# Optimization experiments

Hardware: AMD Instinct MI355X
Metric: run time of the kernel (lower is better)

## Reference

```python
import jax, jax.numpy as jnp
import numpy as np

BATCH, SEQ, IN_DIM, OUT_DIM, N_STATE = 16, 4096, 64, 64, 512


def setup_inputs() -> dict:
    key = jax.random.key(0)
    k_x, k_a, k_b, k_c, k_d = jax.random.split(key, 5)
    x = jax.random.normal(k_x, (BATCH, SEQ, IN_DIM), dtype=jnp.float32)
    # Stable transition matrix: spectral-norm-ish scaling keeps h bounded over SEQ steps.
    A = jax.random.normal(k_a, (N_STATE, N_STATE), dtype=jnp.float32) * (0.9 / np.sqrt(N_STATE))
    B = jax.random.normal(k_b, (N_STATE, IN_DIM), dtype=jnp.float32) / np.sqrt(IN_DIM)
    C = jax.random.normal(k_c, (OUT_DIM, N_STATE), dtype=jnp.float32) / np.sqrt(N_STATE)
    D = jax.random.normal(k_d, (OUT_DIM, IN_DIM), dtype=jnp.float32) / np.sqrt(IN_DIM)
    return {"x": x, "A": A, "B": B, "C": C, "D": D}


def reference(x, A, B, C, D):
    """Linear SSM recurrence: h_t = A h_{t-1} + B x_t ; y_t = C h_t + D x_t.

    x: [batch, seq, in_dim] -> y: [batch, seq, out_dim]
    """
    batch = x.shape[0]
    n = A.shape[0]
    # Precompute input projections once (batched GEMMs outside the scan).
    bx = jnp.einsum("ni,bsi->sbn", B, x)   # [seq, batch, n_state]
    dx = jnp.einsum("oi,bsi->bso", D, x)   # [batch, seq, out_dim]

    def step(h, bx_t):
        # h: [batch, n_state]; bx_t: [batch, n_state]
        h_new = h @ A.T + bx_t
        return h_new, h_new

    h0 = jnp.zeros((batch, n), dtype=x.dtype)
    _, hs = jax.lax.scan(step, h0, bx)      # hs: [seq, batch, n_state]
    y = jnp.einsum("on,sbn->bso", C, hs) + dx
    return y
```

## Files before the change

### kernel.cpp

```cpp
#include <hip/hip_runtime.h>
#include <cstdint>
#include <cstddef>

#define BATCH 16
#define SEQ   4096
#define NS    512
#define TLAG  96
#define CTILE 128
#define XROWS (CTILE + TLAG - 1)
#define XSTR  72
#define BLK   32768

typedef unsigned short u16;
typedef unsigned int   u32;
typedef short bf16x8 __attribute__((ext_vector_type(8)));
typedef float f32x4  __attribute__((ext_vector_type(4)));

__device__ __forceinline__ u16 f2bf(float f) {
    u32 u = __builtin_bit_cast(u32, f);
    return (u16)((u + 0x7FFFu + ((u >> 16) & 1u)) >> 16);
}
__device__ __forceinline__ float bf2f(u16 h) {
    return __builtin_bit_cast(float, (u32)h << 16);
}

__global__ __launch_bounds__(256) void prep_mat(const float* __restrict__ A,
                                                const float* __restrict__ B,
                                                const float* __restrict__ C,
                                                u16* __restrict__ Arm,
                                                u16* __restrict__ At,
                                                u16* __restrict__ Rt,
                                                u16* __restrict__ L)
{
    const int id = blockIdx.x * 256 + threadIdx.x;
    if (id < 262144) {
        const int c = id & 511;
        const u16 v = f2bf(A[id]);
        Arm[id] = v;
        At[(size_t)c * 512 + (id >> 9)] = v;
    } else if (id < 262144 + 32768) {
        const int i = id - 262144;
        Rt[(size_t)(i & 63) * 512 + (i >> 6)] = f2bf(B[i]);
    } else {
        const int i = id - 262144 - 32768;
        L[i] = f2bf(C[i]);
    }
}

__device__ __forceinline__ void gemm_tile(const u16* __restrict__ apM,
                                          const u16* __restrict__ bT, int n0,
                                          u16* __restrict__ oRM,
                                          u16* __restrict__ oT, int rowT,
                                          u16* __restrict__ lds)
{
    const int tid = threadIdx.x;
    const int w = tid >> 6, l = tid & 63;
    const int lr = l & 15, q8 = (l >> 4) * 8;

    const u16* ap  = apM + (size_t)(w * 16 + lr) * NS + q8;
    const u16* bp0 = bT  + (size_t)(n0 + lr) * NS + q8;

    f32x4 acc[4];
    const f32x4 zero = {0.f, 0.f, 0.f, 0.f};
    #pragma unroll
    for (int nt = 0; nt < 4; ++nt) acc[nt] = zero;

    #pragma unroll 4
    for (int ks = 0; ks < 16; ++ks) {
        const bf16x8 a = *(const bf16x8*)(ap + ks * 32);
        #pragma unroll
        for (int nt = 0; nt < 4; ++nt) {
            const bf16x8 bfr = *(const bf16x8*)(bp0 + (size_t)nt * 16 * NS + ks * 32);
            acc[nt] = __builtin_amdgcn_mfma_f32_16x16x32_bf16(a, bfr, acc[nt], 0, 0, 0);
        }
    }

    const int rr = (l >> 4) * 4;
    if (oT) {
        #pragma unroll
        for (int nt = 0; nt < 4; ++nt) {
            const int col = n0 + nt * 16 + lr;
            ushort4 pk;
            pk.x = f2bf(acc[nt][0]); pk.y = f2bf(acc[nt][1]);
            pk.z = f2bf(acc[nt][2]); pk.w = f2bf(acc[nt][3]);
            *(ushort4*)(oT + (size_t)col * NS + rowT + w * 16 + rr) = pk;
        }
    }
    if (oRM) {
        #pragma unroll
        for (int nt = 0; nt < 4; ++nt)
            #pragma unroll
            for (int r = 0; r < 4; ++r)
                lds[(w * 16 + rr + r) * 72 + nt * 16 + lr] = f2bf(acc[nt][r]);
        __syncthreads();
        const int r  = tid >> 2;
        const int c0 = (tid & 3) * 16;
        #pragma unroll
        for (int k = 0; k < 4; ++k) {
            const ushort4 q = *(const ushort4*)&lds[r * 72 + c0 + k * 4];
            *(ushort4*)(oRM + (size_t)r * NS + n0 + c0 + k * 4) = q;
        }
    }
}

__global__ __launch_bounds__(256, 1) void stage_kernel(const u16* __restrict__ expAp,
                                                       const u16* __restrict__ expBT,
                                                       u16* __restrict__ expOut,
                                                       const u16* __restrict__ sqIn,
                                                       const u16* __restrict__ sqInT,
                                                       u16* __restrict__ sqOutRM,
                                                       u16* __restrict__ sqOutT,
                                                       int E)
{
    __shared__ u16 lds[64 * 72];
    const int t = blockIdx.x;
    if (t < E) {
        const int j = t >> 3, n0 = (t & 7) * 64;
        gemm_tile(expAp + (size_t)j * BLK, expBT, n0,
                  expOut + (size_t)j * BLK, nullptr, 0, lds);
    } else {
        const int tt = t - E;
        const int mr = tt >> 3, n0 = (tt & 7) * 64;
        gemm_tile(sqIn + (size_t)mr * BLK, sqInT, n0,
                  sqOutRM + (size_t)mr * BLK, sqOutT, mr * 64, lds);
    }
}

__global__ __launch_bounds__(256, 1) void g_kernel(const u16* __restrict__ Rt,
                                                   const u16* __restrict__ L,
                                                   const float* __restrict__ D,
                                                   u16* __restrict__ Gsw)
{
    __shared__ u16 lds[64 * 72];
    const int m = blockIdx.x;
    const int q = m >> 4, r = m & 15;
    const u16* ap0 = Rt + (size_t)q * BLK;
    const u16* bT0 = L  + (size_t)r * BLK;

    const int tid = threadIdx.x;
    const int w = tid >> 6, l = tid & 63;
    const int lr = l & 15, q8 = (l >> 4) * 8;

    const u16* ap  = ap0 + (size_t)(w * 16 + lr) * NS + q8;
    const u16* bp0 = bT0 + (size_t)lr * NS + q8;

    f32x4 acc[4];
    const f32x4 zero = {0.f, 0.f, 0.f, 0.f};
    #pragma unroll
    for (int nt = 0; nt < 4; ++nt) acc[nt] = zero;

    #pragma unroll 4
    for (int ks = 0; ks < 16; ++ks) {
        const bf16x8 a = *(const bf16x8*)(ap + ks * 32);
        #pragma unroll
        for (int nt = 0; nt < 4; ++nt) {
            const bf16x8 bfr = *(const bf16x8*)(bp0 + (size_t)nt * 16 * NS + ks * 32);
            acc[nt] = __builtin_amdgcn_mfma_f32_16x16x32_bf16(a, bfr, acc[nt], 0, 0, 0);
        }
    }

    const int rr = (l >> 4) * 4;
    #pragma unroll
    for (int nt = 0; nt < 4; ++nt)
        #pragma unroll
        for (int rk = 0; rk < 4; ++rk)
            lds[(nt * 16 + lr) * 72 + (w * 16 + rr + rk)] = f2bf(acc[nt][rk]);
    __syncthreads();

    const int f = tid >> 6;
    #pragma unroll
    for (int f2 = 0; f2 < 8; f2 += 4) {
        const int fi = f2 + f;
        const int ks = fi >> 2, nt = fi & 3;
        const int o  = nt * 16 + (l & 15);
        const int i0 = ks * 32 + (l >> 4) * 8;
        u16 v[8];
        #pragma unroll
        for (int j = 0; j < 8; ++j) {
            u16 gv = lds[o * 72 + i0 + j];
            if (m == 0) gv = f2bf(bf2f(gv) + D[o * 64 + i0 + j]);
            v[j] = gv;
        }
        ushort4 p0; p0.x = v[0]; p0.y = v[1]; p0.z = v[2]; p0.w = v[3];
        ushort4 p1; p1.x = v[4]; p1.y = v[5]; p1.z = v[6]; p1.w = v[7];
        u16* dst = Gsw + ((size_t)(m * 8 + fi) * 64 + l) * 8;
        *(ushort4*)(dst + 0) = p0;
        *(ushort4*)(dst + 4) = p1;
    }
}

__global__ __launch_bounds__(256, 2) void conv_kernel(const float* __restrict__ x,
                                                      const u16* __restrict__ gsw,
                                                      float* __restrict__ y)
{
    __shared__ u16 Xs[XROWS * XSTR];
    __shared__ uint4 Gs[2][1024];

    const int tid = threadIdx.x;
    const int b  = blockIdx.y;
    const int t0 = blockIdx.x * CTILE;

    {
        const int g = tid & 15;
        int r = tid >> 4;
        #pragma unroll
        for (int it = 0; it < 14; ++it, r += 16) {
            if (r < XROWS) {
                const int t = t0 + r - (TLAG - 1);
                ushort4 o;
                if (t < 0) {
                    o.x = 0; o.y = 0; o.z = 0; o.w = 0;
                } else {
                    const float4 v = *(const float4*)(x + ((size_t)b * SEQ + t) * 64 + g * 4);
                    o.x = f2bf(v.x); o.y = f2bf(v.y); o.z = f2bf(v.z); o.w = f2bf(v.w);
                }
                *(ushort4*)&Xs[r * XSTR + g * 4] = o;
            }
        }
    }

    const uint4* gp4 = (const uint4*)gsw;
    uint4 st[4];
    #pragma unroll
    for (int j = 0; j < 4; ++j) st[j] = gp4[tid + j * 256];

    const int w    = tid >> 6;
    const int l    = tid & 63;
    const int lr   = l & 15;
    const int q8   = (l >> 4) * 8;
    const int wrow = w * 32;

    f32x4 acc[2][4];
    const f32x4 zero = {0.f, 0.f, 0.f, 0.f};
    #pragma unroll
    for (int mt = 0; mt < 2; ++mt)
        #pragma unroll
        for (int nt = 0; nt < 4; ++nt) acc[mt][nt] = zero;

    #pragma unroll
    for (int j = 0; j < 4; ++j) Gs[0][tid + j * 256] = st[j];
    __syncthreads();

    for (int p = 0; p < TLAG / 2; ++p) {
        const int cur = p & 1;
        if (p < TLAG / 2 - 1) {
            #pragma unroll
            for (int j = 0; j < 4; ++j) st[j] = gp4[(p + 1) * 1024 + tid + j * 256];
        }
        #pragma unroll
        for (int sub = 0; sub < 2; ++sub) {
            const int m = 2 * p + sub;
            bf16x8 bc[8];
            #pragma unroll
            for (int f = 0; f < 8; ++f)
                bc[f] = __builtin_bit_cast(bf16x8, Gs[cur][sub * 512 + f * 64 + l]);

            const int rbase = wrow + lr + (TLAG - 1) - m;
            bf16x8 a[2][2];
            #pragma unroll
            for (int mt = 0; mt < 2; ++mt)
                #pragma unroll
                for (int ks = 0; ks < 2; ++ks)
                    a[mt][ks] = *(const bf16x8*)&Xs[(rbase + mt * 16) * XSTR + ks * 32 + q8];

            #pragma unroll
            for (int ks = 0; ks < 2; ++ks)
                #pragma unroll
                for (int mt = 0; mt < 2; ++mt)
                    #pragma unroll
                    for (int nt = 0; nt < 4; ++nt)
                        acc[mt][nt] = __builtin_amdgcn_mfma_f32_16x16x32_bf16(
                            a[mt][ks], bc[ks * 4 + nt], acc[mt][nt], 0, 0, 0);
        }
        if (p < TLAG / 2 - 1) {
            #pragma unroll
            for (int j = 0; j < 4; ++j) Gs[cur ^ 1][tid + j * 256] = st[j];
        }
        __syncthreads();
    }

    const int rr = (l >> 4) * 4;
    #pragma unroll
    for (int mt = 0; mt < 2; ++mt) {
        #pragma unroll
        for (int nt = 0; nt < 4; ++nt) {
            const int t = t0 + wrow + mt * 16 + rr;
            const int o = nt * 16 + lr;
            float* yp = y + ((size_t)b * SEQ + t) * 64 + o;
            #pragma unroll
            for (int r = 0; r < 4; ++r) yp[(size_t)r * 64] = acc[mt][nt][r];
        }
    }
}

extern "C" void kernel_launch(void* const* d_in, const int* in_sizes, int n_in,
                              void* d_out, int out_size, void* d_ws, size_t ws_size,
                              hipStream_t stream)
{
    const float* x = (const float*)d_in[0];
    const float* A = (const float*)d_in[1];
    const float* B = (const float*)d_in[2];
    const float* C = (const float*)d_in[3];
    const float* D = (const float*)d_in[4];
    float* y = (float*)d_out;

    char* w = (char*)d_ws;
    u16* Arm   = (u16*)(w + 8650752);
    u16* At    = (u16*)(w + 9175040);
    u16* A2rm  = (u16*)(w + 9699328);
    u16* A2t   = (u16*)(w + 10223616);
    u16* A4rm  = (u16*)(w + 10747904);
    u16* A4t   = (u16*)(w + 11272192);
    u16* A8rm  = (u16*)(w + 11796480);
    u16* A8t   = (u16*)(w + 12320768);
    u16* A16rm = (u16*)(w + 12845056);
    u16* A16t  = (u16*)(w + 13369344);
    u16* A32rm = (u16*)(w + 13893632);
    u16* A32t  = (u16*)(w + 14417920);
    u16* A64rm = (u16*)(w + 14942208);
    u16* L     = (u16*)(w + 15532032);
    u16* Rt    = (u16*)(w + 16580608);
    u16* Gsw   = (u16*)(w + 17104896);

    prep_mat<<<1280, 256, 0, stream>>>(A, B, C, Arm, At, Rt, L);

    stage_kernel<<<72, 256, 0, stream>>>(L, At, L + 1 * BLK,
                                         Arm, At, A2rm, A2t, 8);
    stage_kernel<<<80, 256, 0, stream>>>(L, A2t, L + 2 * BLK,
                                         A2rm, A2t, A4rm, A4t, 16);
    stage_kernel<<<96, 256, 0, stream>>>(L, A4t, L + 4 * BLK,
                                         A4rm, A4t, A8rm, A8t, 32);
    stage_kernel<<<128, 256, 0, stream>>>(L, A8t, L + 8 * BLK,
                                          A8rm, A8t, A16rm, A16t, 64);
    stage_kernel<<<72, 256, 0, stream>>>(Rt, A16rm, Rt + 1 * BLK,
                                         A16rm, A16t, A32rm, A32t, 8);
    stage_kernel<<<80, 256, 0, stream>>>(Rt, A32rm, Rt + 2 * BLK,
                                         A32rm, A32t, A64rm, nullptr, 16);
    stage_kernel<<<16, 256, 0, stream>>>(Rt, A64rm, Rt + 4 * BLK,
                                         nullptr, nullptr, nullptr, nullptr, 16);
    g_kernel<<<TLAG, 256, 0, stream>>>(Rt, L, D, Gsw);

    conv_kernel<<<dim3(SEQ / CTILE, BATCH), 256, 0, stream>>>(x, Gsw, y);
}
```

Baseline: 217.7 us.

## Split conv lag taps across warps and reduce partial sums through LDS

The conv kernel now gives each warp a quarter of the lag taps across the whole 128-row tile, instead of a quarter of the rows across all taps. Each warp reads its own filter slices straight from global memory, which removes the shared double-buffered filter staging and the per-step block barriers. The four per-warp partial sums are then reduced through two LDS buffers, which alias the input tile, before a coalesced store. In exchange each warp holds 128 accumulator registers, which risks register pressure or spills at two blocks per CU, and the final reduction adds shared-memory traffic and extra barriers.

```diff
diff --git a/kernel.cpp b/kernel.cpp
--- a/kernel.cpp
+++ b/kernel.cpp
@@ -10,6 +10,7 @@
 #define XROWS (CTILE + TLAG - 1)
 #define XSTR  72
 #define BLK   32768
+#define RSTR  66
 
 typedef unsigned short u16;
 typedef unsigned int   u32;
@@ -193,8 +194,10 @@
                                                       const u16* __restrict__ gsw,
                                                       float* __restrict__ y)
 {
-    __shared__ u16 Xs[XROWS * XSTR];
-    __shared__ uint4 Gs[2][1024];
+    __shared__ __align__(16) char smem[67584];
+    u16*   Xs   = (u16*)smem;
+    float* buf0 = (float*)smem;
+    float* buf1 = (float*)(smem + 33792);
 
     const int tid = threadIdx.x;
     const int b  = blockIdx.y;
@@ -218,77 +221,74 @@
             }
         }
     }
+    __syncthreads();
+
+    const int w  = tid >> 6;
+    const int l  = tid & 63;
+    const int lr = l & 15;
+    const int q8 = (l >> 4) * 8;
+
+    f32x4 acc[8][4];
+    const f32x4 zero = {0.f, 0.f, 0.f, 0.f};
+    #pragma unroll
+    for (int mt = 0; mt < 8; ++mt)
+        #pragma unroll
+        for (int nt = 0; nt < 4; ++nt) acc[mt][nt] = zero;
 
     const uint4* gp4 = (const uint4*)gsw;
-    uint4 st[4];
-    #pragma unroll
-    for (int j = 0; j < 4; ++j) st[j] = gp4[tid + j * 256];
-
-    const int w    = tid >> 6;
-    const int l    = tid & 63;
-    const int lr   = l & 15;
-    const int q8   = (l >> 4) * 8;
-    const int wrow = w * 32;
-
-    f32x4 acc[2][4];
-    const f32x4 zero = {0.f, 0.f, 0.f, 0.f};
-    #pragma unroll
-    for (int mt = 0; mt < 2; ++mt)
-        #pragma unroll
-        for (int nt = 0; nt < 4; ++nt) acc[mt][nt] = zero;
-
-    #pragma unroll
-    for (int j = 0; j < 4; ++j) Gs[0][tid + j * 256] = st[j];
-    __syncthreads();
-
-    for (int p = 0; p < TLAG / 2; ++p) {
-        const int cur = p & 1;
-        if (p < TLAG / 2 - 1) {
-            #pragma unroll
-            for (int j = 0; j < 4; ++j) st[j] = gp4[(p + 1) * 1024 + tid + j * 256];
-        }
-        #pragma unroll
-        for (int sub = 0; sub < 2; ++sub) {
-            const int m = 2 * p + sub;
-            bf16x8 bc[8];
-            #pragma unroll
-            for (int f = 0; f < 8; ++f)
-                bc[f] = __builtin_bit_cast(bf16x8, Gs[cur][sub * 512 + f * 64 + l]);
-
-            const int rbase = wrow + lr + (TLAG - 1) - m;
-            bf16x8 a[2][2];
-            #pragma unroll
-            for (int mt = 0; mt < 2; ++mt)
+
+    for (int i = 0; i < TLAG / 4; ++i) {
+        const int m = w * (TLAG / 4) + i;
+
+        bf16x8 bc[8];
+        #pragma unroll
+        for (int f = 0; f < 8; ++f)
+            bc[f] = __builtin_bit_cast(bf16x8, gp4[(size_t)m * 512 + f * 64 + l]);
+
+        const int rbase = lr + (TLAG - 1) - m;
+        #pragma unroll
+        for (int mt = 0; mt < 8; ++mt) {
+            const bf16x8 a0 = *(const bf16x8*)&Xs[(rbase + mt * 16) * XSTR + q8];
+            const bf16x8 a1 = *(const bf16x8*)&Xs[(rbase + mt * 16) * XSTR + 32 + q8];
+            #pragma unroll
+            for (int nt = 0; nt < 4; ++nt)
+                acc[mt][nt] = __builtin_amdgcn_mfma_f32_16x16x32_bf16(a0, bc[nt], acc[mt][nt], 0, 0, 0);
+            #pragma unroll
+            for (int nt = 0; nt < 4; ++nt)
+                acc[mt][nt] = __builtin_amdgcn_mfma_f32_16x16x32_bf16(a1, bc[4 + nt], acc[mt][nt], 0, 0, 0);
+        }
+    }
+    __syncthreads();
+
+    const int rr = (l >> 4) * 4;
+    if (w < 2) {
+        float* bf = w ? buf1 : buf0;
+        #pragma unroll
+        for (int mt = 0; mt < 8; ++mt)
+            #pragma unroll
+            for (int nt = 0; nt < 4; ++nt)
                 #pragma unroll
-                for (int ks = 0; ks < 2; ++ks)
-                    a[mt][ks] = *(const bf16x8*)&Xs[(rbase + mt * 16) * XSTR + ks * 32 + q8];
-
-            #pragma unroll
-            for (int ks = 0; ks < 2; ++ks)
+                for (int r = 0; r < 4; ++r)
+                    bf[(mt * 16 + rr + r) * RSTR + nt * 16 + lr] = acc[mt][nt][r];
+    }
+    __syncthreads();
+    if (w >= 2) {
+        float* bf = (w == 2) ? buf0 : buf1;
+        #pragma unroll
+        for (int mt = 0; mt < 8; ++mt)
+            #pragma unroll
+            for (int nt = 0; nt < 4; ++nt)
                 #pragma unroll
-                for (int mt = 0; mt < 2; ++mt)
-                    #pragma unroll
-                    for (int nt = 0; nt < 4; ++nt)
-                        acc[mt][nt] = __builtin_amdgcn_mfma_f32_16x16x32_bf16(
-                            a[mt][ks], bc[ks * 4 + nt], acc[mt][nt], 0, 0, 0);
-        }
-        if (p < TLAG / 2 - 1) {
-            #pragma unroll
-            for (int j = 0; j < 4; ++j) Gs[cur ^ 1][tid + j * 256] = st[j];
-        }
-        __syncthreads();
-    }
-
-    const int rr = (l >> 4) * 4;
-    #pragma unroll
-    for (int mt = 0; mt < 2; ++mt) {
-        #pragma unroll
-        for (int nt = 0; nt < 4; ++nt) {
-            const int t = t0 + wrow + mt * 16 + rr;
-            const int o = nt * 16 + lr;
-            float* yp = y + ((size_t)b * SEQ + t) * 64 + o;
-            #pragma unroll
-            for (int r = 0; r < 4; ++r) yp[(size_t)r * 64] = acc[mt][nt][r];
+                for (int r = 0; r < 4; ++r)
+                    bf[(mt * 16 + rr + r) * RSTR + nt * 16 + lr] += acc[mt][nt][r];
+    }
+    __syncthreads();
+    {
+        float* yp = y + ((size_t)b * SEQ + t0 + 32 * w) * 64 + l;
+        #pragma unroll 4
+        for (int i = 0; i < 32; ++i) {
+            const int row = 32 * w + i;
+            yp[(size_t)i * 64] = buf0[row * RSTR + l] + buf1[row * RSTR + l];
         }
     }
 }
```

Result: faster. 210.2 us (-3.5%).
